# Performance work log

Hardware: AMD Instinct MI355X
Metric: run time of the kernel (lower is better)

Reference implementation:

```python
import jax, jax.numpy as jnp
import numpy as np

B, N, C = 4, 8192, 256
E = 262144
OUT = 256  # out_ch * heads = 128 * 2


def setup_inputs() -> dict:
    key = jax.random.key(0)
    ks = jax.random.split(key, 6)
    x = jax.random.normal(ks[0], (B, N, C), dtype=jnp.float32)
    edge_index = jax.random.randint(ks[1], (2, E), 0, N, dtype=jnp.int64)
    s = 1.0 / np.sqrt(C)
    W_self = jax.random.normal(ks[2], (C, OUT), dtype=jnp.float32) * s
    b_self = jax.random.normal(ks[3], (OUT,), dtype=jnp.float32) * 0.01
    W_neigh = jax.random.normal(ks[4], (C, OUT), dtype=jnp.float32) * s
    b_neigh = jax.random.normal(ks[5], (OUT,), dtype=jnp.float32) * 0.01
    return {"x": x, "edge_index": edge_index, "W_self": W_self, "b_self": b_self,
            "W_neigh": W_neigh, "b_neigh": b_neigh}


def _build_A_hat(edge_index, n):
    # A[i,j] = multiplicity of edge (src=i, dst=j), plus self loops (identity),
    # matching torch.sparse_coo_tensor(...).to_dense() which sums duplicates.
    src, dst = edge_index[0], edge_index[1]
    A = jnp.zeros((n, n), dtype=jnp.float32).at[src, dst].add(1.0)
    A = A + jnp.eye(n, dtype=jnp.float32)
    deg = jnp.clip(A.sum(axis=1), 1.0, None)  # [N]
    return A / deg[:, None]  # row-normalized adjacency


def reference(x, edge_index, W_self, b_self, W_neigh, b_neigh):
    n = x.shape[1]
    A_hat = _build_A_hat(edge_index, n)            # [N, N]
    h_self = x @ W_self + b_self                   # [B, N, OUT]
    y = jnp.einsum('ij,bjc->bic', A_hat, x)        # neighbor aggregation
    h_nei = y @ W_neigh + b_neigh                  # [B, N, OUT]
    return jax.nn.gelu(h_self + h_nei, approximate=False)
```

## Files before the change

kernel.cpp:

```cpp
#include <hip/hip_runtime.h>
#include <math.h>

#define BB 4
#define NN 8192
#define CC 256
#define OUTC 256
#define EE 262144
#define MROWS (BB*NN)
#define CAP 96

typedef __attribute__((ext_vector_type(8))) short short8;
typedef __attribute__((ext_vector_type(4))) short s16x4;
typedef __attribute__((ext_vector_type(4))) float f32x4;
typedef __attribute__((ext_vector_type(2))) unsigned int u32x2;

__device__ inline unsigned short f2bf(float f) {
    union { float f; unsigned u; } a; a.f = f;
    unsigned u = a.u;
    u += 0x7fffu + ((u >> 16) & 1u);
    return (unsigned short)(u >> 16);
}
__device__ inline float bf2f(unsigned short h) {
    union { unsigned u; float f; } a; a.u = ((unsigned)h) << 16;
    return a.f;
}
__device__ inline float asf(unsigned u) {
    union { unsigned u; float f; } a; a.u = u;
    return a.f;
}
__device__ inline float gelu1(float v) {
    float t = v * (0.7978845608f + 0.0356774081f * v * v);
    float e = __expf(2.0f * t);
    float th = 1.0f - 2.0f / (e + 1.0f);
    return 0.5f * v * (1.0f + th);
}


__global__ __launch_bounds__(256) void prep_w(const float* __restrict__ Ws,
                                              const float* __restrict__ Wn,
                                              unsigned short* __restrict__ Wt2,
                                              int* __restrict__ cnt) {
    int bi = blockIdx.x;
    int tid = threadIdx.x;
    if (bi >= 32) {
        cnt[(bi - 32) * 256 + tid] = 0;
        return;
    }
    __shared__ float tile[64][65];
    int kt = bi >> 3, nt = bi & 7;
    int k0 = kt * 64, n0 = nt * 64;
    const float* W = (n0 < 256) ? Ws : Wn;
    int ncol = n0 & 255;
#pragma unroll
    for (int p = 0; p < 4; p++) {
        int krow = p * 16 + (tid >> 4);
        int col = (tid & 15) * 4;
        float4 v = *(const float4*)&W[(size_t)(k0 + krow) * 256 + ncol + col];
        tile[krow][col + 0] = v.x;
        tile[krow][col + 1] = v.y;
        tile[krow][col + 2] = v.z;
        tile[krow][col + 3] = v.w;
    }
    __syncthreads();
#pragma unroll
    for (int e = 0; e < 2; e++) {
        int idx = e * 256 + tid;
        int lane = idx & 63;
        int ni = (idx >> 6) & 3;
        int kkl = idx >> 8;
        int kk = kt * 2 + kkl;
        int qrow = lane >> 4, fr = lane & 15;
        short8 t;
#pragma unroll
        for (int j = 0; j < 8; j++)
            t[j] = (short)f2bf(tile[kkl * 32 + qrow * 8 + j][ni * 16 + fr]);
        *(short8*)&Wt2[(size_t)(((nt * 8 + kk) * 4 + ni) * 512) + lane * 8] = t;
    }
}


#define APAD 8
#define ALD (256 + APAD)

__global__ __launch_bounds__(256, 2) void gemm_fill(const float* __restrict__ X,
                                                    const unsigned short* __restrict__ Wt2,
                                                    unsigned short* __restrict__ Zb,
                                                    unsigned short* __restrict__ U,
                                                    const int* __restrict__ ei,
                                                    int* __restrict__ cnt,
                                                    unsigned short* __restrict__ adjb) {
    __shared__ unsigned short sA[64 * ALD];
    int bi = blockIdx.x;
    int tid = threadIdx.x;

    if (bi < 256) {
        int e = bi * 256 + tid;
        for (; e < EE; e += 256 * 256) {
            int s = ei[e] & (NN - 1);
            int d = ei[EE + e] & (NN - 1);
            int slot = atomicAdd(&cnt[s], 1);
            if (slot < CAP) adjb[(size_t)s * CAP + slot] = (unsigned short)d;
        }
        return;
    }

    int wave = tid >> 6, lane = tid & 63;
    int row0 = (bi - 256) * 64;
    int qrow = lane >> 4;
    int fr = lane & 15;

#pragma unroll
    for (int q = 0; q < 16; q++) {
        int f = q * 1024 + tid * 4;
        int rr = f >> 8, k0 = f & 255;
        float4 v = *(const float4*)&X[(size_t)(row0 + rr) * 256 + k0];
        s16x4 t;
        t[0] = (short)f2bf(v.x); t[1] = (short)f2bf(v.y);
        t[2] = (short)f2bf(v.z); t[3] = (short)f2bf(v.w);
        *(s16x4*)&sA[rr * ALD + k0] = t;
    }
    __syncthreads();

#pragma unroll 1
    for (int sp = 0; sp < 2; sp++) {
        int colbase = wave * 128 + sp * 64;
        int ct = wave * 2 + sp;
        const unsigned short* Bp = Wt2 + (size_t)ct * 8 * 4 * 512 + lane * 8;

        f32x4 acc[4][4];
#pragma unroll
        for (int ni = 0; ni < 4; ni++)
#pragma unroll
            for (int mi = 0; mi < 4; mi++) acc[ni][mi] = (f32x4)0.0f;

        short8 bbuf[3][4];
#pragma unroll
        for (int ni = 0; ni < 4; ni++) {
            bbuf[0][ni] = *(const short8*)&Bp[(size_t)(0 * 4 + ni) * 512];
            bbuf[1][ni] = *(const short8*)&Bp[(size_t)(1 * 4 + ni) * 512];
        }

#pragma unroll
        for (int kk = 0; kk < 8; kk++) {
            if (kk < 6) {
#pragma unroll
                for (int ni = 0; ni < 4; ni++)
                    bbuf[(kk + 2) % 3][ni] =
                        *(const short8*)&Bp[(size_t)((kk + 2) * 4 + ni) * 512];
            }
            int ak = kk * 32 + qrow * 8;
            short8 af[4];
#pragma unroll
            for (int mi = 0; mi < 4; mi++)
                af[mi] = *(const short8*)&sA[(mi * 16 + fr) * ALD + ak];
#pragma unroll
            for (int ni = 0; ni < 4; ni++)
#pragma unroll
                for (int mi = 0; mi < 4; mi++)
                    acc[ni][mi] = __builtin_amdgcn_mfma_f32_16x16x32_bf16(
                        bbuf[kk % 3][ni], af[mi], acc[ni][mi], 0, 0, 0);
        }

#pragma unroll
        for (int mi = 0; mi < 4; mi++) {
            size_t row = (size_t)(row0 + mi * 16 + fr);
#pragma unroll
            for (int ni = 0; ni < 4; ni++) {
                int col = colbase + ni * 16 + qrow * 4;
                s16x4 t;
                t[0] = (short)f2bf(acc[ni][mi][0]);
                t[1] = (short)f2bf(acc[ni][mi][1]);
                t[2] = (short)f2bf(acc[ni][mi][2]);
                t[3] = (short)f2bf(acc[ni][mi][3]);
                if (colbase < 256) *(s16x4*)&Zb[row * 512 + 256 + col] = t;
                else               *(s16x4*)&U[row * 256 + (col - 256)] = t;
            }
        }
    }
}


__global__ __launch_bounds__(256) void agg_gelu(const unsigned short* __restrict__ U,
                                                const int* __restrict__ cnt,
                                                const unsigned short* __restrict__ adjb,
                                                const float* __restrict__ bs,
                                                const float* __restrict__ bn,
                                                float* __restrict__ Out) {
    int r = blockIdx.x & 7;
    int q = blockIdx.x >> 3;
    int b = r & 3;
    int g = ((r >> 2) << 10) + q;
    int i = (g << 2) + (threadIdx.x >> 6);
    i = __builtin_amdgcn_readfirstlane(i);
    int lane = threadIdx.x & 63;
    int c = lane * 4;

    const unsigned short* Ub = U + (size_t)b * NN * 256;
    size_t row = (size_t)b * NN + i;

    int deg = cnt[i];
    int m = min(deg, CAP);
    const unsigned* lp = (const unsigned*)(adjb + (size_t)i * CAP);

    unsigned w[16];
#pragma unroll
    for (int t = 0; t < 16; t++) w[t] = lp[t];

    const unsigned* ZbP = (const unsigned*)Out;
    u32x2 zz = __builtin_nontemporal_load((const u32x2*)&ZbP[row * 256 + 128 + (c >> 1)]);
    float4 vs = *(const float4*)&bs[c];
    float4 vn = *(const float4*)&bn[c];
    u32x2 sv = *(const u32x2*)(Ub + (size_t)i * 256 + c);

    u32x2 v[32];
#pragma unroll
    for (int t = 0; t < 32; t++) {
        unsigned jw = w[t >> 1];
        unsigned j = (t & 1) ? (jw >> 16) : (jw & 0xffffu);
        j = (t < m) ? j : (unsigned)i;
        v[t] = *(const u32x2*)(Ub + (size_t)j * 256 + c);
    }
    __builtin_amdgcn_sched_barrier(0);

    float a0 = asf(sv[0] << 16), a1 = asf(sv[0] & 0xffff0000u);
    float a2 = asf(sv[1] << 16), a3 = asf(sv[1] & 0xffff0000u);
#pragma unroll
    for (int t = 0; t < 32; t++) {
        unsigned msk = (t < m) ? 0xffffffffu : 0u;
        unsigned lo = v[t][0] & msk, hi = v[t][1] & msk;
        a0 += asf(lo << 16); a1 += asf(lo & 0xffff0000u);
        a2 += asf(hi << 16); a3 += asf(hi & 0xffff0000u);
    }

    int p = 32;
    while (p < m) {
        u32x2 tv[16];
#pragma unroll
        for (int t = 0; t < 16; t++) {
            int s2 = p + t;
            unsigned jw = lp[s2 >> 1];
            unsigned j = (s2 & 1) ? (jw >> 16) : (jw & 0xffffu);
            j = (s2 < m) ? j : (unsigned)i;
            tv[t] = *(const u32x2*)(Ub + (size_t)j * 256 + c);
        }
        __builtin_amdgcn_sched_barrier(0);
#pragma unroll
        for (int t = 0; t < 16; t++) {
            unsigned msk = (p + t < m) ? 0xffffffffu : 0u;
            unsigned lo = tv[t][0] & msk, hi = tv[t][1] & msk;
            a0 += asf(lo << 16); a1 += asf(lo & 0xffff0000u);
            a2 += asf(hi << 16); a3 += asf(hi & 0xffff0000u);
        }
        p += 16;
    }

    float z0 = bf2f((unsigned short)(zz[0] & 0xffff));
    float z1 = bf2f((unsigned short)(zz[0] >> 16));
    float z2 = bf2f((unsigned short)(zz[1] & 0xffff));
    float z3 = bf2f((unsigned short)(zz[1] >> 16));

    float s = 1.0f / (float)(1 + deg);
    float v0 = z0 + vs.x + vn.x + s * a0;
    float v1 = z1 + vs.y + vn.y + s * a1;
    float v2 = z2 + vs.z + vn.z + s * a2;
    float v3 = z3 + vs.w + vn.w + s * a3;

    f32x4 gout;
    gout[0] = gelu1(v0);
    gout[1] = gelu1(v1);
    gout[2] = gelu1(v2);
    gout[3] = gelu1(v3);
    __builtin_nontemporal_store(gout, (f32x4*)&Out[row * 256 + c]);
}


extern "C" void kernel_launch(void* const* d_in, const int* in_sizes, int n_in,
                              void* d_out, int out_size, void* d_ws, size_t ws_size,
                              hipStream_t stream) {
    const float* x   = (const float*)d_in[0];
    const int* ei    = (const int*)d_in[1];
    const float* Ws  = (const float*)d_in[2];
    const float* bsv = (const float*)d_in[3];
    const float* Wn  = (const float*)d_in[4];
    const float* bnv = (const float*)d_in[5];
    float* out = (float*)d_out;

    char* ws = (char*)d_ws;
    size_t o = 0;
    unsigned short* U   = (unsigned short*)(ws + o); o += (size_t)MROWS * OUTC * 2;
    unsigned short* Wt2 = (unsigned short*)(ws + o); o += (size_t)512 * 256 * 2;
    int* cnt = (int*)(ws + o);  o += (size_t)NN * 4;
    unsigned short* adjb = (unsigned short*)(ws + o); o += (size_t)NN * CAP * 2;

    prep_w<<<64, 256, 0, stream>>>(Ws, Wn, Wt2, cnt);

    gemm_fill<<<768, 256, 0, stream>>>(x, Wt2, (unsigned short*)out, U, ei, cnt, adjb);

    agg_gelu<<<8192, 256, 0, stream>>>(U, cnt, adjb, bsv, bnv, out);
}
```

Before: 158.5 us.

## Split wave into half-waves gathering two neighbors with 16-byte loads

The aggregation kernel now has each half-wave gather a different neighbor row with 16-byte loads covering 8 channels per lane, instead of the whole wave reading one row with 8-byte loads. Partial sums are combined with a cross-half shuffle. The self term is folded in via a mask, and the loop runs over neighbor pairs in chunks of 8 instead of a fixed 32-way unrolled prefetch. This is meant to widen memory transactions and halve the serial gather depth, at the cost of extra shuffles, more accumulator registers and a less aggressive prefetch.

```diff
diff --git a/kernel.cpp b/kernel.cpp
--- a/kernel.cpp
+++ b/kernel.cpp
@@ -13,6 +13,7 @@
 typedef __attribute__((ext_vector_type(4))) short s16x4;
 typedef __attribute__((ext_vector_type(4))) float f32x4;
 typedef __attribute__((ext_vector_type(2))) unsigned int u32x2;
+typedef __attribute__((ext_vector_type(4))) unsigned int u32x4;
 
 __device__ inline unsigned short f2bf(float f) {
     union { float f; unsigned u; } a; a.f = f;
@@ -193,66 +194,79 @@
     int i = (g << 2) + (threadIdx.x >> 6);
     i = __builtin_amdgcn_readfirstlane(i);
     int lane = threadIdx.x & 63;
-    int c = lane * 4;
+    int l5 = lane & 31;
+    int sub = lane >> 5;
+    int cb = l5 * 8;
+    int c_out = cb + sub * 4;
 
     const unsigned short* Ub = U + (size_t)b * NN * 256;
     size_t row = (size_t)b * NN + i;
 
     int deg = cnt[i];
     int m = min(deg, CAP);
+    int P = m & 1;
+    int K = (m + 1) >> 1;
     const unsigned* lp = (const unsigned*)(adjb + (size_t)i * CAP);
 
-    unsigned w[16];
-#pragma unroll
-    for (int t = 0; t < 16; t++) w[t] = lp[t];
-
     const unsigned* ZbP = (const unsigned*)Out;
-    u32x2 zz = __builtin_nontemporal_load((const u32x2*)&ZbP[row * 256 + 128 + (c >> 1)]);
-    float4 vs = *(const float4*)&bs[c];
-    float4 vn = *(const float4*)&bn[c];
-    u32x2 sv = *(const u32x2*)(Ub + (size_t)i * 256 + c);
-
-    u32x2 v[32];
-#pragma unroll
-    for (int t = 0; t < 32; t++) {
-        unsigned jw = w[t >> 1];
-        unsigned j = (t & 1) ? (jw >> 16) : (jw & 0xffffu);
-        j = (t < m) ? j : (unsigned)i;
-        v[t] = *(const u32x2*)(Ub + (size_t)j * 256 + c);
-    }
-    __builtin_amdgcn_sched_barrier(0);
-
-    float a0 = asf(sv[0] << 16), a1 = asf(sv[0] & 0xffff0000u);
-    float a2 = asf(sv[1] << 16), a3 = asf(sv[1] & 0xffff0000u);
-#pragma unroll
-    for (int t = 0; t < 32; t++) {
-        unsigned msk = (t < m) ? 0xffffffffu : 0u;
-        unsigned lo = v[t][0] & msk, hi = v[t][1] & msk;
-        a0 += asf(lo << 16); a1 += asf(lo & 0xffff0000u);
-        a2 += asf(hi << 16); a3 += asf(hi & 0xffff0000u);
-    }
-
-    int p = 32;
-    while (p < m) {
-        u32x2 tv[16];
-#pragma unroll
-        for (int t = 0; t < 16; t++) {
-            int s2 = p + t;
-            unsigned jw = lp[s2 >> 1];
-            unsigned j = (s2 & 1) ? (jw >> 16) : (jw & 0xffffu);
-            j = (s2 < m) ? j : (unsigned)i;
-            tv[t] = *(const u32x2*)(Ub + (size_t)j * 256 + c);
-        }
-        __builtin_amdgcn_sched_barrier(0);
-#pragma unroll
-        for (int t = 0; t < 16; t++) {
-            unsigned msk = (p + t < m) ? 0xffffffffu : 0u;
-            unsigned lo = tv[t][0] & msk, hi = tv[t][1] & msk;
-            a0 += asf(lo << 16); a1 += asf(lo & 0xffff0000u);
-            a2 += asf(hi << 16); a3 += asf(hi & 0xffff0000u);
-        }
-        p += 16;
-    }
+    u32x2 zz = __builtin_nontemporal_load((const u32x2*)&ZbP[row * 256 + 128 + (c_out >> 1)]);
+    float4 vs = *(const float4*)&bs[c_out];
+    float4 vn = *(const float4*)&bn[c_out];
+    u32x4 sv4 = *(const u32x4*)(Ub + (size_t)i * 256 + cb);
+
+    float a[8];
+    unsigned smask = (sub == 0 && P == 0) ? 0xffffffffu : 0u;
+#pragma unroll
+    for (int d = 0; d < 4; d++) {
+        unsigned x = sv4[d] & smask;
+        a[2 * d]     = asf(x << 16);
+        a[2 * d + 1] = asf(x & 0xffff0000u);
+    }
+
+    int p = 0;
+    for (; p + 8 <= K; p += 8) {
+        unsigned w[8];
+#pragma unroll
+        for (int t = 0; t < 8; t++) w[t] = lp[p + t];
+        u32x4 v4[8];
+#pragma unroll
+        for (int t = 0; t < 8; t++) {
+            unsigned lo = w[t] & 0xffffu;
+            unsigned hi = w[t] >> 16;
+            hi = (2 * (p + t) + 1 < m) ? hi : (unsigned)i;
+            unsigned j = sub ? hi : lo;
+            v4[t] = *(const u32x4*)(Ub + (size_t)j * 256 + cb);
+        }
+#pragma unroll
+        for (int t = 0; t < 8; t++) {
+#pragma unroll
+            for (int d = 0; d < 4; d++) {
+                a[2 * d]     += asf(v4[t][d] << 16);
+                a[2 * d + 1] += asf(v4[t][d] & 0xffff0000u);
+            }
+        }
+    }
+    for (; p < K; p++) {
+        unsigned w = lp[p];
+        unsigned lo = w & 0xffffu;
+        unsigned hi = w >> 16;
+        hi = (2 * p + 1 < m) ? hi : (unsigned)i;
+        unsigned j = sub ? hi : lo;
+        u32x4 v4 = *(const u32x4*)(Ub + (size_t)j * 256 + cb);
+#pragma unroll
+        for (int d = 0; d < 4; d++) {
+            a[2 * d]     += asf(v4[d] << 16);
+            a[2 * d + 1] += asf(v4[d] & 0xffff0000u);
+        }
+    }
+
+#pragma unroll
+    for (int k = 0; k < 8; k++) a[k] += __shfl_xor(a[k], 32);
+
+    float r0 = sub ? a[4] : a[0];
+    float r1 = sub ? a[5] : a[1];
+    float r2 = sub ? a[6] : a[2];
+    float r3 = sub ? a[7] : a[3];
 
     float z0 = bf2f((unsigned short)(zz[0] & 0xffff));
     float z1 = bf2f((unsigned short)(zz[0] >> 16));
@@ -260,17 +274,17 @@
     float z3 = bf2f((unsigned short)(zz[1] >> 16));
 
     float s = 1.0f / (float)(1 + deg);
-    float v0 = z0 + vs.x + vn.x + s * a0;
-    float v1 = z1 + vs.y + vn.y + s * a1;
-    float v2 = z2 + vs.z + vn.z + s * a2;
-    float v3 = z3 + vs.w + vn.w + s * a3;
+    float v0 = z0 + vs.x + vn.x + s * r0;
+    float v1 = z1 + vs.y + vn.y + s * r1;
+    float v2 = z2 + vs.z + vn.z + s * r2;
+    float v3 = z3 + vs.w + vn.w + s * r3;
 
     f32x4 gout;
     gout[0] = gelu1(v0);
     gout[1] = gelu1(v1);
     gout[2] = gelu1(v2);
     gout[3] = gelu1(v3);
-    __builtin_nontemporal_store(gout, (f32x4*)&Out[row * 256 + c]);
+    __builtin_nontemporal_store(gout, (f32x4*)&Out[row * 256 + c_out]);
 }
 
 
```

New measurement: 143.5 us. -9.5%, faster.
